# Kernel tuning notes

Measured on AMD Instinct MI355X. Metric: run time of the kernel, lower is better.

## Reference

```python
import jax, jax.numpy as jnp
import numpy as np

B, T_NEW, D_MODEL, H, DH = 8, 512, 1024, 16, 64
CACHED = 2048
T_TOTAL = CACHED + T_NEW  # static padded total length (last batch item is full)


def setup_inputs() -> dict:
    key = jax.random.key(0)
    ks = jax.random.split(key, 16)
    x_new = jax.random.normal(ks[0], (B, T_NEW, D_MODEL), jnp.float32)
    past_lengths = jax.random.randint(ks[1], (B,), CACHED // 2, CACHED)
    past_lengths = past_lengths.at[-1].set(CACHED).astype(jnp.int32)
    new_counts = jax.random.randint(ks[2], (B,), 1, T_NEW)
    new_counts = new_counts.at[-1].set(T_NEW).astype(jnp.int32)
    # prefix (left-aligned) valid mask for new tokens, matching how the torch
    # module compacts k_new[b, :, :count] into the cache
    valid_new_mask = jnp.arange(T_NEW)[None, :] < new_counts[:, None]
    total_lengths = past_lengths + new_counts
    key_padding_mask = jnp.arange(T_TOTAL)[None, :] < total_lengths[:, None]
    inv_freq = 1.0 / (10000.0 ** (jnp.arange(0, DH, 2, dtype=jnp.float32) / DH))
    pm = (jnp.arange(CACHED)[None, :] < past_lengths[:, None])[:, None, :, None]
    past_k = jax.random.normal(ks[3], (B, H, CACHED, DH), jnp.float32) * pm
    past_v = jax.random.normal(ks[4], (B, H, CACHED, DH), jnp.float32) * pm
    s = 0.02
    Wq = jax.random.normal(ks[5], (D_MODEL, D_MODEL), jnp.float32) * s
    Wk = jax.random.normal(ks[6], (D_MODEL, D_MODEL), jnp.float32) * s
    Wv = jax.random.normal(ks[7], (D_MODEL, D_MODEL), jnp.float32) * s
    Wo = jax.random.normal(ks[8], (D_MODEL, D_MODEL), jnp.float32) * s
    bq = jnp.zeros((D_MODEL,), jnp.float32)
    bk = jnp.zeros((D_MODEL,), jnp.float32)
    bv = jnp.zeros((D_MODEL,), jnp.float32)
    bo = jnp.zeros((D_MODEL,), jnp.float32)
    return {
        'x_new': x_new, 'inv_freq': inv_freq, 'past_k': past_k, 'past_v': past_v,
        'Wq': Wq, 'bq': bq, 'Wk': Wk, 'bk': bk, 'Wv': Wv, 'bv': bv, 'Wo': Wo, 'bo': bo,
        'key_padding_mask': key_padding_mask, 'past_lengths': past_lengths,
        'valid_new_mask': valid_new_mask,
    }


def _rotate_half(x):
    h = x.shape[-1] // 2
    return jnp.concatenate([-x[..., h:], x[..., :h]], axis=-1)


def reference(x_new, inv_freq, past_k, past_v, Wq, bq, Wk, bk, Wv, bv, Wo, bo,
              key_padding_mask, past_lengths, valid_new_mask):
    Bb, Tn, _ = x_new.shape
    # projections -> [B, H, T_new, DH]
    q = (x_new @ Wq.T + bq).reshape(Bb, Tn, H, DH).transpose(0, 2, 1, 3)
    k_new = (x_new @ Wk.T + bk).reshape(Bb, Tn, H, DH).transpose(0, 2, 1, 3)
    v_new = (x_new @ Wv.T + bv).reshape(Bb, Tn, H, DH).transpose(0, 2, 1, 3)
    # RoPE at absolute positions past_len + step (invalid -> 0)
    steps = jnp.arange(Tn)
    positions = jnp.where(valid_new_mask, past_lengths[:, None] + steps[None, :], 0)
    freqs = positions[..., None].astype(jnp.float32) * inv_freq  # [B, T, DH/2]
    emb = jnp.concatenate([freqs, freqs], axis=-1)
    cos = jnp.cos(emb)[:, None].astype(q.dtype)  # [B, 1, T, DH]
    sin = jnp.sin(emb)[:, None].astype(q.dtype)
    q = q * cos + _rotate_half(q) * sin
    k_new = k_new * cos + _rotate_half(k_new) * sin
    vm = valid_new_mask[:, None, :, None].astype(q.dtype)
    q = q * vm
    k_new = k_new * vm
    v_new = v_new * vm
    # zero cached entries past each item's cached length (matches padded cache)
    pm = (jnp.arange(CACHED)[None, :] < past_lengths[:, None])[:, None, :, None]
    past_k = past_k * pm.astype(past_k.dtype)
    past_v = past_v * pm.astype(past_v.dtype)
    # ragged append: scatter new tokens at [past_len, past_len+count); invalid
    # tokens dumped into an extra slot T_TOTAL that is sliced off
    pos_idx = jnp.where(valid_new_mask, past_lengths[:, None] + steps[None, :], T_TOTAL)
    pad = lambda p: jnp.pad(p, ((0, 0), (0, 0), (0, T_TOTAL + 1 - CACHED), (0, 0)))
    scat = jax.vmap(lambda base, new, idx: base.at[:, idx, :].add(new))
    k_total = scat(pad(past_k), k_new, pos_idx)[:, :, :T_TOTAL]
    v_total = scat(pad(past_v), v_new, pos_idx)[:, :, :T_TOTAL]
    # padded SDPA with key-padding mask
    scores = jnp.einsum('bhqd,bhkd->bhqk', q, k_total) / jnp.sqrt(jnp.asarray(DH, q.dtype))
    scores = jnp.where(key_padding_mask[:, None, None, :], scores, jnp.finfo(scores.dtype).min)
    attn = jax.nn.softmax(scores, axis=-1)
    ctx = jnp.einsum('bhqk,bhkd->bhqd', attn, v_total)
    ctx = ctx.transpose(0, 2, 1, 3).reshape(Bb, Tn, D_MODEL)
    out = (ctx @ Wo.T + bo) * valid_new_mask[..., None].astype(ctx.dtype)
    total_lengths = past_lengths + valid_new_mask.sum(axis=1).astype(past_lengths.dtype)
    return out, k_total, v_total, total_lengths
```

## Files before the change

### kernel.cpp

```cpp
#include <hip/hip_runtime.h>
#include <math.h>

#define B_ 8
#define TN 512
#define DM 1024
#define H_ 16
#define DH 64
#define CACHED_ 2048
#define TT 2560

#define QSC 0.18033688011112042f

typedef __attribute__((ext_vector_type(8))) short bf16x8;
typedef __attribute__((ext_vector_type(4))) float f32x4;

union U16x8 { uint4 u; unsigned short s[8]; };
union U16x4 { uint2 u; unsigned short s[4]; };
union F4 { float4 v; float f[4]; };

__device__ __forceinline__ unsigned short f2b(float x) {
    unsigned u = __float_as_uint(x);
    unsigned r = (u + 0x7FFFu + ((u >> 16) & 1u)) >> 16;
    return (unsigned short)r;
}
__device__ __forceinline__ float b2f(unsigned short v) {
    return __uint_as_float((unsigned)v << 16);
}

__device__ __forceinline__ unsigned cvt_pk_bf16(float lo, float hi) {
    unsigned r;
    asm("v_cvt_pk_bf16_f32 %0, %1, %2" : "=v"(r) : "v"(lo), "v"(hi));
    return r;
}

__device__ __forceinline__ void gload16(const void* g, void* l) {
    __builtin_amdgcn_global_load_lds(
        (const __attribute__((address_space(1))) void*)g,
        (__attribute__((address_space(3))) void*)l, 16, 0, 0);
}

__global__ void cvt_all(const float* __restrict__ x,
                        const float* __restrict__ Wq,
                        const float* __restrict__ Wk,
                        const float* __restrict__ Wv,
                        const float* __restrict__ Wo,
                        unsigned short* __restrict__ Xbf,
                        unsigned short* __restrict__ Wqkvb,
                        unsigned short* __restrict__ Wob,
                        const unsigned char* __restrict__ vnm,
                        const unsigned char* __restrict__ kpm,
                        const int* __restrict__ past_len,
                        int* __restrict__ counts,
                        float* __restrict__ total_out) {
    if (blockIdx.x >= 4096) {
        int b = blockIdx.x - 4096;
        __shared__ int red[256];
        int esz = (kpm[1] | kpm[2] | kpm[3]) ? 1 : 4;
        int s = 0;
        for (int t = threadIdx.x; t < TN; t += 256)
            s += (vnm[(size_t)(b * TN + t) * esz] != 0) ? 1 : 0;
        red[threadIdx.x] = s;
        __syncthreads();
        for (int off = 128; off > 0; off >>= 1) {
            if (threadIdx.x < off) red[threadIdx.x] += red[threadIdx.x + off];
            __syncthreads();
        }
        if (threadIdx.x == 0) {
            counts[b] = red[0];
            total_out[b] = (float)(past_len[b] + red[0]);
        }
        return;
    }
    int i8 = (blockIdx.x * 256 + threadIdx.x) << 3;
    const float* src;
    unsigned short* dst;
    int off;
    if (i8 < (1 << 22)) {
        src = x; off = i8; dst = Xbf + i8;
    } else if (i8 < (1 << 22) + (3 << 20)) {
        int j = i8 - (1 << 22);
        int w = j >> 20;
        src = w == 0 ? Wq : (w == 1 ? Wk : Wv);
        off = j & 0xFFFFF;
        dst = Wqkvb + j;
    } else {
        int j = i8 - ((1 << 22) + (3 << 20));
        src = Wo; off = j; dst = Wob + j;
    }
    float4 a = *(const float4*)(src + off);
    float4 b = *(const float4*)(src + off + 4);
    U16x8 o;
    o.s[0] = f2b(a.x); o.s[1] = f2b(a.y); o.s[2] = f2b(a.z); o.s[3] = f2b(a.w);
    o.s[4] = f2b(b.x); o.s[5] = f2b(b.y); o.s[6] = f2b(b.z); o.s[7] = f2b(b.w);
    *(uint4*)dst = o.u;
}

__device__ __forceinline__ void gemm_core(
    const unsigned short* __restrict__ A, const unsigned short* __restrict__ Bw,
    int K, int m0, int n0, short* As2, short* Bs2, f32x4 acc[4][4]) {
    const int tid = threadIdx.x;
    const int wave = tid >> 6, lane = tid & 63;
    const int wm = wave >> 1, wn = wave & 1;
    const int l15 = lane & 15, lq = lane >> 4;

    const int srow = wave * 16 + (lane >> 2);
    const int sc = (lane & 3) << 3;
    const unsigned short* Ag0 = A + (size_t)(m0 + srow) * K + sc;
    const unsigned short* Ag1 = A + (size_t)(m0 + 64 + srow) * K + sc;
    const unsigned short* Bg0 = Bw + (size_t)(n0 + srow) * K + sc;
    const unsigned short* Bg1 = Bw + (size_t)(n0 + 64 + srow) * K + sc;
    const int d0 = wave * 512;
    const int d1 = 2048 + wave * 512;

    gload16(Ag0, As2 + d0);
    gload16(Ag1, As2 + d1);
    gload16(Bg0, Bs2 + d0);
    gload16(Bg1, Bs2 + d1);

    int cur = 0;
    for (int k0 = 0; k0 < K; k0 += 32) {
        asm volatile("s_waitcnt vmcnt(0)" ::: "memory");
        __builtin_amdgcn_s_barrier();

        int kn = (k0 + 32 < K) ? k0 + 32 : k0;
        short* An = As2 + ((cur ^ 1) << 12);
        short* Bn = Bs2 + ((cur ^ 1) << 12);
        gload16(Ag0 + kn, An + d0);
        gload16(Ag1 + kn, An + d1);
        gload16(Bg0 + kn, Bn + d0);
        gload16(Bg1 + kn, Bn + d1);

        const short* Ac = As2 + (cur << 12);
        const short* Bc = Bs2 + (cur << 12);
        bf16x8 af[4], bf[4];
#pragma unroll
        for (int mi = 0; mi < 4; ++mi)
            af[mi] = *(const bf16x8*)&Ac[(wm * 64 + mi * 16 + l15) * 32 + lq * 8];
#pragma unroll
        for (int ni = 0; ni < 4; ++ni)
            bf[ni] = *(const bf16x8*)&Bc[(wn * 64 + ni * 16 + l15) * 32 + lq * 8];
#pragma unroll
        for (int mi = 0; mi < 4; ++mi)
#pragma unroll
            for (int ni = 0; ni < 4; ++ni)
                acc[mi][ni] = __builtin_amdgcn_mfma_f32_16x16x32_bf16(
                    af[mi], bf[ni], acc[mi][ni], 0, 0, 0);
        cur ^= 1;
    }
}

__global__ __launch_bounds__(256) void gemm_qkv_mfma(
    const unsigned short* __restrict__ Xbf,
    const unsigned short* __restrict__ Wqkv,
    const float* __restrict__ bq, const float* __restrict__ bk,
    const float* __restrict__ bv, const float* __restrict__ inv_freq,
    const int* __restrict__ past_len,
    unsigned short* __restrict__ Qraw, unsigned short* __restrict__ Kraw,
    unsigned short* __restrict__ Vraw) {
    __shared__ __align__(16) short As[2 * 128 * 32];
    __shared__ __align__(16) short Bs[2 * 128 * 32];
    f32x4 acc[4][4] = {};
    const int m0 = blockIdx.y << 7, n0 = blockIdx.x << 7;
    gemm_core(Xbf, Wqkv, DM, m0, n0, As, Bs, acc);

    const int which = n0 >> 10;
    const int tid = threadIdx.x, wave = tid >> 6, lane = tid & 63;
    const int wm = wave >> 1, wn = wave & 1, l15 = lane & 15, lq = lane >> 4;

    if (which == 0) {
        const int bb = m0 >> 9;
        const int pl = past_len[bb];
        const int hh = (n0 + wn * 64) >> 6;
#pragma unroll
        for (int ni = 0; ni < 2; ++ni) {
            int i = ni * 16 + l15;
            int n1 = n0 + wn * 64 + ni * 16 + l15;
            float fi = inv_freq[i];
            float blo = bq[n1], bhi = bq[n1 + 32];
#pragma unroll
            for (int mi = 0; mi < 4; ++mi) {
#pragma unroll
                for (int r = 0; r < 4; ++r) {
                    int m = m0 + wm * 64 + mi * 16 + lq * 4 + r;
                    int t = m & 511;
                    float ang = (float)(pl + t) * fi;
                    float s, c;
                    __sincosf(ang, &s, &c);
                    float x1 = acc[mi][ni][r] + blo;
                    float x2 = acc[mi][ni + 2][r] + bhi;
                    size_t base = ((size_t)(bb * H_ + hh) * TN + t) * DH;
                    Qraw[base + i]      = f2b((x1 * c - x2 * s) * QSC);
                    Qraw[base + i + 32] = f2b((x2 * c + x1 * s) * QSC);
                }
            }
        }
    } else {
        const float* bias = which == 1 ? bk : bv;
        unsigned short* dst = which == 1 ? Kraw : Vraw;
#pragma unroll
        for (int ni = 0; ni < 4; ++ni) {
            int n1 = (n0 & 1023) + wn * 64 + ni * 16 + l15;
            float bb = bias[n1];
            int h = n1 >> 6, dh = n1 & 63;
#pragma unroll
            for (int mi = 0; mi < 4; ++mi) {
#pragma unroll
                for (int r = 0; r < 4; ++r) {
                    int m = m0 + wm * 64 + mi * 16 + lq * 4 + r;
                    int b = m >> 9, t = m & 511;
                    dst[((size_t)(b * H_ + h) * TN + t) * DH + dh] =
                        f2b(acc[mi][ni][r] + bb);
                }
            }
        }
    }
}

__global__ __launch_bounds__(256) void gemm_out_mfma(
    const unsigned short* __restrict__ Ctxb,
    const unsigned short* __restrict__ Wob,
    const float* __restrict__ bo, const int* __restrict__ counts,
    float* __restrict__ Out) {
    __shared__ __align__(16) short As[2 * 128 * 32];
    __shared__ __align__(16) short Bs[2 * 128 * 32];
    f32x4 acc[4][4] = {};
    const int m0 = blockIdx.y << 7, n0 = blockIdx.x << 7;
    gemm_core(Ctxb, Wob, DM, m0, n0, As, Bs, acc);

    const int tid = threadIdx.x, wave = tid >> 6, lane = tid & 63;
    const int wm = wave >> 1, wn = wave & 1, l15 = lane & 15, lq = lane >> 4;
    const int cnt = counts[m0 >> 9];
#pragma unroll
    for (int mi = 0; mi < 4; ++mi) {
#pragma unroll
        for (int r = 0; r < 4; ++r) {
            int m = m0 + wm * 64 + mi * 16 + lq * 4 + r;
            int t = m & 511;
            bool valid = t < cnt;
#pragma unroll
            for (int ni = 0; ni < 4; ++ni) {
                int n = n0 + wn * 64 + ni * 16 + l15;
                Out[(size_t)m * DM + n] = valid ? acc[mi][ni][r] + bo[n] : 0.f;
            }
        }
    }
}

__global__ void build_kv(const float* __restrict__ past_k,
                         const float* __restrict__ past_v,
                         const unsigned short* __restrict__ Kraw,
                         const unsigned short* __restrict__ Vraw,
                         const float* __restrict__ inv_freq,
                         const int* __restrict__ past_len,
                         const int* __restrict__ counts,
                         float* __restrict__ Ko, float* __restrict__ Vo,
                         unsigned short* __restrict__ Kb16,
                         unsigned short* __restrict__ Vb16) {
    int idx = blockIdx.x * 256 + threadIdx.x;
    int i = idx & 7;
    int p = idx >> 3;
    int h = blockIdx.y, bz = blockIdx.z;
    int pl = past_len[bz], cnt = counts[bz];
    int dh = i << 2;
    size_t obase = ((size_t)(bz * H_ + h) * TT + p) * DH;
    F4 k1, k2, v1, v2;
    if (p < pl) {
        size_t ib = ((size_t)(bz * H_ + h) * CACHED_ + p) * DH;
        k1.v = *(const float4*)(past_k + ib + dh);
        k2.v = *(const float4*)(past_k + ib + dh + 32);
        v1.v = *(const float4*)(past_v + ib + dh);
        v2.v = *(const float4*)(past_v + ib + dh + 32);
    } else if (p < pl + cnt) {
        int t = p - pl;
        size_t ib = ((size_t)(bz * H_ + h) * TN + t) * DH;
        U16x4 ka, kc, va, vc;
        ka.u = *(const uint2*)(Kraw + ib + dh);
        kc.u = *(const uint2*)(Kraw + ib + dh + 32);
        va.u = *(const uint2*)(Vraw + ib + dh);
        vc.u = *(const uint2*)(Vraw + ib + dh + 32);
#pragma unroll
        for (int j = 0; j < 4; ++j) {
            float ang = (float)p * inv_freq[dh + j];
            float s, c;
            __sincosf(ang, &s, &c);
            float x1 = b2f(ka.s[j]), x2 = b2f(kc.s[j]);
            k1.f[j] = x1 * c - x2 * s;
            k2.f[j] = x2 * c + x1 * s;
            v1.f[j] = b2f(va.s[j]);
            v2.f[j] = b2f(vc.s[j]);
        }
    } else {
        k1.v = k2.v = v1.v = v2.v = make_float4(0.f, 0.f, 0.f, 0.f);
    }
    *(float4*)(Ko + obase + dh) = k1.v;
    *(float4*)(Ko + obase + dh + 32) = k2.v;
    *(float4*)(Vo + obase + dh) = v1.v;
    *(float4*)(Vo + obase + dh + 32) = v2.v;
    U16x4 o;
#pragma unroll
    for (int j = 0; j < 4; ++j) o.s[j] = f2b(k1.f[j]);
    *(uint2*)(Kb16 + obase + dh) = o.u;
#pragma unroll
    for (int j = 0; j < 4; ++j) o.s[j] = f2b(k2.f[j]);
    *(uint2*)(Kb16 + obase + dh + 32) = o.u;
#pragma unroll
    for (int j = 0; j < 4; ++j) o.s[j] = f2b(v1.f[j]);
    *(uint2*)(Vb16 + obase + dh) = o.u;
#pragma unroll
    for (int j = 0; j < 4; ++j) o.s[j] = f2b(v2.f[j]);
    *(uint2*)(Vb16 + obase + dh + 32) = o.u;
}

__global__ __launch_bounds__(512) void attn_mfma(
    const unsigned short* __restrict__ Qbf,
    const unsigned short* __restrict__ Kb,
    const unsigned short* __restrict__ Vb,
    const int* __restrict__ past_len, const int* __restrict__ counts,
    unsigned short* __restrict__ Ctxb) {
    const int j = blockIdx.x;
    const int xcd = j & 7;
    const int tloc = j >> 3;
    const int qt = tloc & 3;
    const int p = ((tloc >> 2) << 3) | xcd;
    const int b = p >> 4, h = p & 15;

    const int tid = threadIdx.x;
    const int wave = tid >> 6, lane = tid & 63;
    const int l15 = lane & 15, lq = lane >> 4;

    __shared__ __align__(16) short Qs[8192];
    __shared__ __align__(16) short Ks[2][4096];
    __shared__ __align__(16) short Vt[4096];
    __shared__ __align__(16) short Pb[8192];

    const size_t qbase = ((size_t)(b * H_ + h) * TN + qt * 128) * DH;
    const size_t kbase = (size_t)(b * H_ + h) * TT * DH;

    const int total = past_len[b] + counts[b];
    const int ntiles = (total + 63) >> 6;

    const int dA = tid;
    const int krA = (dA >> 7) * 16 + ((dA & 15) ^ ((dA >> 4) & 7));
    const int kcA = ((dA >> 4) & 7) << 3;
    const unsigned short* KgA = Kb + kbase + (size_t)krA * DH + kcA;
    const int kdoffA = wave * 512;

    gload16(KgA, &Ks[0][kdoffA]);

    const int kp = tid & 31;
    const int dh4 = (tid >> 5) << 2;
    const int kc = kp >> 2, ko2 = (kp & 3) << 1;
    const unsigned short* Vg = Vb + kbase + (size_t)(2 * kp) * DH + dh4;
    uint2 vr0 = *(const uint2*)Vg;
    uint2 vr1 = *(const uint2*)(Vg + DH);

#pragma unroll
    for (int jj = 0; jj < 2; ++jj) {
        int e = tid + (jj << 9);
        int row = e >> 3, c = e & 7;
        *(uint4*)&Qs[(((row >> 4) * 8 + c) * 16 + ((row & 15) ^ c)) * 8] =
            *(const uint4*)(Qbf + qbase + row * 64 + c * 8);
    }
    __syncthreads();
    const int c0 = lq, c1 = 4 + lq;
    bf16x8 qa0 = *(const bf16x8*)&Qs[((wave * 8 + c0) * 16 + (l15 ^ c0)) * 8];
    bf16x8 qa1 = *(const bf16x8*)&Qs[((wave * 8 + c1) * 16 + (l15 ^ c1)) * 8];

    float rsum[4] = {0.f, 0.f, 0.f, 0.f};
    f32x4 O[4] = {};
    unsigned short* Pw = (unsigned short*)(Pb + wave * 1024);
    const int pc0 = l15 >> 3, pwo = l15 & 7;

    int cur = 0;
    for (int kt = 0; kt < ntiles; ++kt) {
        asm volatile("s_waitcnt vmcnt(0)" ::: "memory");
        __builtin_amdgcn_s_barrier();

        {
            U16x4 a, cc;
            a.u = vr0;
            cc.u = vr1;
#pragma unroll
            for (int jj = 0; jj < 4; ++jj) {
                int dh = dh4 + jj;
                unsigned pk = (unsigned)a.s[jj] | ((unsigned)cc.s[jj] << 16);
                *(unsigned*)&Vt[((((dh >> 4) * 8 + kc) * 16) + ((dh & 15) ^ kc)) * 8 + ko2] = pk;
            }
        }
        {
            int ktn = (kt + 1 < ntiles) ? kt + 1 : kt;
            gload16(KgA + (size_t)ktn * 64 * DH, &Ks[cur ^ 1][kdoffA]);
            vr0 = *(const uint2*)(Vg + (size_t)ktn * 64 * DH);
            vr1 = *(const uint2*)(Vg + (size_t)ktn * 64 * DH + DH);
        }

        asm volatile("s_waitcnt lgkmcnt(0)" ::: "memory");
        __builtin_amdgcn_s_barrier();
        __builtin_amdgcn_sched_barrier(0);

        const short* Kcur = Ks[cur];
        f32x4 S[4];
        __builtin_amdgcn_s_setprio(1);
#pragma unroll
        for (int nt = 0; nt < 4; ++nt) {
            f32x4 acc = {};
            bf16x8 kb0 = *(const bf16x8*)&Kcur[((nt * 8 + c0) * 16 + (l15 ^ c0)) * 8];
            acc = __builtin_amdgcn_mfma_f32_16x16x32_bf16(qa0, kb0, acc, 0, 0, 0);
            bf16x8 kb1 = *(const bf16x8*)&Kcur[((nt * 8 + c1) * 16 + (l15 ^ c1)) * 8];
            acc = __builtin_amdgcn_mfma_f32_16x16x32_bf16(qa1, kb1, acc, 0, 0, 0);
            S[nt] = acc;
        }
        __builtin_amdgcn_s_setprio(0);

        int limit = total - (kt << 6);
        if (limit < 64) {
#pragma unroll
            for (int nt = 0; nt < 4; ++nt) {
                bool ok = nt * 16 + l15 < limit;
#pragma unroll
                for (int r = 0; r < 4; ++r) S[nt][r] = ok ? S[nt][r] : -1e30f;
            }
        }

#pragma unroll
        for (int nt = 0; nt < 4; ++nt) {
            const int pc = nt * 2 + pc0;
#pragma unroll
            for (int rr = 0; rr < 2; ++rr) {
                float p0 = __builtin_amdgcn_exp2f(S[nt][2 * rr]);
                float p1 = __builtin_amdgcn_exp2f(S[nt][2 * rr + 1]);
                rsum[2 * rr] += p0;
                rsum[2 * rr + 1] += p1;
                unsigned pk = cvt_pk_bf16(p0, p1);
                int row0 = lq * 4 + 2 * rr;
                int row1 = row0 + 1;
                Pw[(pc * 16 + (row0 ^ pc)) * 8 + pwo] = (unsigned short)pk;
                Pw[(pc * 16 + (row1 ^ pc)) * 8 + pwo] = (unsigned short)(pk >> 16);
            }
        }
        asm volatile("s_waitcnt lgkmcnt(0)" ::: "memory");

        bf16x8 pa0 = *(const bf16x8*)&Pw[(c0 * 16 + (l15 ^ c0)) * 8];
        bf16x8 pa1 = *(const bf16x8*)&Pw[(c1 * 16 + (l15 ^ c1)) * 8];
        __builtin_amdgcn_s_setprio(1);
#pragma unroll
        for (int nt = 0; nt < 4; ++nt) {
            bf16x8 vb0 = *(const bf16x8*)&Vt[((nt * 8 + c0) * 16 + (l15 ^ c0)) * 8];
            O[nt] = __builtin_amdgcn_mfma_f32_16x16x32_bf16(pa0, vb0, O[nt], 0, 0, 0);
            bf16x8 vb1 = *(const bf16x8*)&Vt[((nt * 8 + c1) * 16 + (l15 ^ c1)) * 8];
            O[nt] = __builtin_amdgcn_mfma_f32_16x16x32_bf16(pa1, vb1, O[nt], 0, 0, 0);
        }
        __builtin_amdgcn_s_setprio(0);
        cur ^= 1;
    }

#pragma unroll
    for (int off = 1; off < 16; off <<= 1)
#pragma unroll
        for (int r = 0; r < 4; ++r) rsum[r] += __shfl_xor(rsum[r], off);

#pragma unroll
    for (int r = 0; r < 4; ++r) {
        float inv = 1.f / rsum[r];
        int t = qt * 128 + wave * 16 + lq * 4 + r;
        size_t mbase = ((size_t)(b * TN + t)) * DM + h * DH;
#pragma unroll
        for (int nt = 0; nt < 4; ++nt)
            Ctxb[mbase + nt * 16 + l15] = f2b(O[nt][r] * inv);
    }
}

extern "C" void kernel_launch(void* const* d_in, const int* in_sizes, int n_in,
                              void* d_out, int out_size, void* d_ws, size_t ws_size,
                              hipStream_t stream) {
    const float* x_new    = (const float*)d_in[0];
    const float* inv_freq = (const float*)d_in[1];
    const float* past_k   = (const float*)d_in[2];
    const float* past_v   = (const float*)d_in[3];
    const float* Wq = (const float*)d_in[4];
    const float* bq = (const float*)d_in[5];
    const float* Wk = (const float*)d_in[6];
    const float* bk = (const float*)d_in[7];
    const float* Wv = (const float*)d_in[8];
    const float* bv = (const float*)d_in[9];
    const float* Wo = (const float*)d_in[10];
    const float* bo = (const float*)d_in[11];
    const unsigned char* kpm = (const unsigned char*)d_in[12];
    const int* past_len      = (const int*)d_in[13];
    const unsigned char* vnm = (const unsigned char*)d_in[14];

    float* out      = (float*)d_out;
    float* k_total  = out + (size_t)B_ * TN * DM;
    float* v_total  = k_total + (size_t)B_ * H_ * TT * DH;
    float* total_out = v_total + (size_t)B_ * H_ * TT * DH;

    const size_t NQ = (size_t)B_ * TN * DM;
    const size_t NKV = (size_t)B_ * H_ * TT * DH;

    int* counts = (int*)d_ws;
    unsigned short* Xbf   = (unsigned short*)((char*)d_ws + 256);
    unsigned short* Wqkvb = Xbf + NQ;
    unsigned short* Wob   = Wqkvb + (size_t)3 * DM * DM;
    unsigned short* Qraw  = Wob + (size_t)DM * DM;
    unsigned short* Kraw  = Qraw + NQ;
    unsigned short* Vraw  = Kraw + NQ;
    unsigned short* Ctxb  = Vraw + NQ;
    unsigned short* Kb16  = Ctxb + NQ;
    unsigned short* Vb16  = Kb16 + NKV;

    cvt_all<<<4104, 256, 0, stream>>>(x_new, Wq, Wk, Wv, Wo, Xbf, Wqkvb, Wob,
                                      vnm, kpm, past_len, counts, total_out);

    gemm_qkv_mfma<<<dim3(24, 32), 256, 0, stream>>>(
        Xbf, Wqkvb, bq, bk, bv, inv_freq, past_len, Qraw, Kraw, Vraw);
    build_kv<<<dim3((TT * 8) / 256, H_, B_), 256, 0, stream>>>(
        past_k, past_v, Kraw, Vraw, inv_freq, past_len, counts,
        k_total, v_total, Kb16, Vb16);
    attn_mfma<<<512, 512, 0, stream>>>(Qraw, Kb16, Vb16,
                                       past_len, counts, Ctxb);
    gemm_out_mfma<<<dim3(8, 32), 256, 0, stream>>>(Ctxb, Wob, bo, counts, out);
}
```

Baseline: 496.9 us.

## Split attention over KV halves and merge partial results in a separate kernel

Attention now splits each (batch, head, q-tile) across two blocks, each handling half of the KV tiles, and writes unnormalized fp32 partial outputs and row sums to workspace. A new merge kernel sums the two partials, normalizes, and writes the bf16 context. The aim is to double the block count and balance ragged sequence lengths across CUs. The Q and P shared buffers are merged to cut LDS use, launch bounds now request higher occupancy, and the setprio hints are dropped. The cost is extra fp32 global traffic and one more kernel launch. Merging without a running max is valid only because scores are not max-subtracted, the same as in the code before.

```diff
diff --git a/kernel.cpp b/kernel.cpp
--- a/kernel.cpp
+++ b/kernel.cpp
@@ -10,6 +10,8 @@
 #define TT 2560
 
 #define QSC 0.18033688011112042f
+#define OHALF 4194304
+#define RHALF 65536
 
 typedef __attribute__((ext_vector_type(8))) short bf16x8;
 typedef __attribute__((ext_vector_type(4))) float f32x4;
@@ -311,33 +313,38 @@
     *(uint2*)(Vb16 + obase + dh + 32) = o.u;
 }
 
-__global__ __launch_bounds__(512) void attn_mfma(
+__global__ __launch_bounds__(512, 8) void attn_split(
     const unsigned short* __restrict__ Qbf,
     const unsigned short* __restrict__ Kb,
     const unsigned short* __restrict__ Vb,
     const int* __restrict__ past_len, const int* __restrict__ counts,
-    unsigned short* __restrict__ Ctxb) {
+    float* __restrict__ Opart,
+    float* __restrict__ Rpart) {
     const int j = blockIdx.x;
     const int xcd = j & 7;
-    const int tloc = j >> 3;
-    const int qt = tloc & 3;
-    const int p = ((tloc >> 2) << 3) | xcd;
+    const int sub = (j >> 3) & 7;
+    const int qt = sub & 3;
+    const int half = sub >> 2;
+    const int pg = j >> 6;
+    const int p = pg * 8 + xcd;
     const int b = p >> 4, h = p & 15;
 
     const int tid = threadIdx.x;
     const int wave = tid >> 6, lane = tid & 63;
     const int l15 = lane & 15, lq = lane >> 4;
 
-    __shared__ __align__(16) short Qs[8192];
     __shared__ __align__(16) short Ks[2][4096];
     __shared__ __align__(16) short Vt[4096];
-    __shared__ __align__(16) short Pb[8192];
+    __shared__ __align__(16) short PQ[8192];
 
     const size_t qbase = ((size_t)(b * H_ + h) * TN + qt * 128) * DH;
     const size_t kbase = (size_t)(b * H_ + h) * TT * DH;
 
     const int total = past_len[b] + counts[b];
     const int ntiles = (total + 63) >> 6;
+    const int nth = (ntiles + 1) >> 1;
+    const int kt0 = half * nth;
+    const int kt1 = (kt0 + nth < ntiles) ? kt0 + nth : ntiles;
 
     const int dA = tid;
     const int krA = (dA >> 7) * 16 + ((dA & 15) ^ ((dA >> 4) & 7));
@@ -345,34 +352,34 @@
     const unsigned short* KgA = Kb + kbase + (size_t)krA * DH + kcA;
     const int kdoffA = wave * 512;
 
-    gload16(KgA, &Ks[0][kdoffA]);
+    gload16(KgA + (size_t)kt0 * 64 * DH, &Ks[0][kdoffA]);
 
     const int kp = tid & 31;
     const int dh4 = (tid >> 5) << 2;
     const int kc = kp >> 2, ko2 = (kp & 3) << 1;
     const unsigned short* Vg = Vb + kbase + (size_t)(2 * kp) * DH + dh4;
-    uint2 vr0 = *(const uint2*)Vg;
-    uint2 vr1 = *(const uint2*)(Vg + DH);
+    uint2 vr0 = *(const uint2*)(Vg + (size_t)kt0 * 64 * DH);
+    uint2 vr1 = *(const uint2*)(Vg + (size_t)kt0 * 64 * DH + DH);
 
 #pragma unroll
     for (int jj = 0; jj < 2; ++jj) {
         int e = tid + (jj << 9);
         int row = e >> 3, c = e & 7;
-        *(uint4*)&Qs[(((row >> 4) * 8 + c) * 16 + ((row & 15) ^ c)) * 8] =
+        *(uint4*)&PQ[(((row >> 4) * 8 + c) * 16 + ((row & 15) ^ c)) * 8] =
             *(const uint4*)(Qbf + qbase + row * 64 + c * 8);
     }
     __syncthreads();
     const int c0 = lq, c1 = 4 + lq;
-    bf16x8 qa0 = *(const bf16x8*)&Qs[((wave * 8 + c0) * 16 + (l15 ^ c0)) * 8];
-    bf16x8 qa1 = *(const bf16x8*)&Qs[((wave * 8 + c1) * 16 + (l15 ^ c1)) * 8];
+    bf16x8 qa0 = *(const bf16x8*)&PQ[((wave * 8 + c0) * 16 + (l15 ^ c0)) * 8];
+    bf16x8 qa1 = *(const bf16x8*)&PQ[((wave * 8 + c1) * 16 + (l15 ^ c1)) * 8];
 
     float rsum[4] = {0.f, 0.f, 0.f, 0.f};
     f32x4 O[4] = {};
-    unsigned short* Pw = (unsigned short*)(Pb + wave * 1024);
+    unsigned short* Pw = (unsigned short*)(PQ + wave * 1024);
     const int pc0 = l15 >> 3, pwo = l15 & 7;
 
     int cur = 0;
-    for (int kt = 0; kt < ntiles; ++kt) {
+    for (int kt = kt0; kt < kt1; ++kt) {
         asm volatile("s_waitcnt vmcnt(0)" ::: "memory");
         __builtin_amdgcn_s_barrier();
 
@@ -388,7 +395,7 @@
             }
         }
         {
-            int ktn = (kt + 1 < ntiles) ? kt + 1 : kt;
+            int ktn = (kt + 1 < kt1) ? kt + 1 : kt;
             gload16(KgA + (size_t)ktn * 64 * DH, &Ks[cur ^ 1][kdoffA]);
             vr0 = *(const uint2*)(Vg + (size_t)ktn * 64 * DH);
             vr1 = *(const uint2*)(Vg + (size_t)ktn * 64 * DH + DH);
@@ -400,7 +407,6 @@
 
         const short* Kcur = Ks[cur];
         f32x4 S[4];
-        __builtin_amdgcn_s_setprio(1);
 #pragma unroll
         for (int nt = 0; nt < 4; ++nt) {
             f32x4 acc = {};
@@ -410,7 +416,6 @@
             acc = __builtin_amdgcn_mfma_f32_16x16x32_bf16(qa1, kb1, acc, 0, 0, 0);
             S[nt] = acc;
         }
-        __builtin_amdgcn_s_setprio(0);
 
         int limit = total - (kt << 6);
         if (limit < 64) {
@@ -442,7 +447,6 @@
 
         bf16x8 pa0 = *(const bf16x8*)&Pw[(c0 * 16 + (l15 ^ c0)) * 8];
         bf16x8 pa1 = *(const bf16x8*)&Pw[(c1 * 16 + (l15 ^ c1)) * 8];
-        __builtin_amdgcn_s_setprio(1);
 #pragma unroll
         for (int nt = 0; nt < 4; ++nt) {
             bf16x8 vb0 = *(const bf16x8*)&Vt[((nt * 8 + c0) * 16 + (l15 ^ c0)) * 8];
@@ -450,7 +454,6 @@
             bf16x8 vb1 = *(const bf16x8*)&Vt[((nt * 8 + c1) * 16 + (l15 ^ c1)) * 8];
             O[nt] = __builtin_amdgcn_mfma_f32_16x16x32_bf16(pa1, vb1, O[nt], 0, 0, 0);
         }
-        __builtin_amdgcn_s_setprio(0);
         cur ^= 1;
     }
 
@@ -459,15 +462,42 @@
 #pragma unroll
         for (int r = 0; r < 4; ++r) rsum[r] += __shfl_xor(rsum[r], off);
 
+    float* Od = Opart + (size_t)half * OHALF;
+    float* Rd = Rpart + (size_t)half * RHALF;
 #pragma unroll
     for (int r = 0; r < 4; ++r) {
-        float inv = 1.f / rsum[r];
         int t = qt * 128 + wave * 16 + lq * 4 + r;
-        size_t mbase = ((size_t)(b * TN + t)) * DM + h * DH;
+        size_t obase = ((size_t)(b * H_ + h) * TN + t) * DH;
 #pragma unroll
         for (int nt = 0; nt < 4; ++nt)
-            Ctxb[mbase + nt * 16 + l15] = f2b(O[nt][r] * inv);
-    }
+            Od[obase + nt * 16 + l15] = O[nt][r];
+        if (l15 == 0) Rd[(size_t)(b * H_ + h) * TN + t] = rsum[r];
+    }
+}
+
+__global__ __launch_bounds__(256) void attn_merge(
+    const float* __restrict__ Opart, const float* __restrict__ Rpart,
+    unsigned short* __restrict__ Ctxb) {
+    int idx = blockIdx.x * 256 + threadIdx.x;
+    int i8 = idx & 7;
+    int row = idx >> 3;
+    int dh8 = i8 << 3;
+    const float* O0 = Opart + (size_t)row * DH + dh8;
+    const float* O1 = O0 + OHALF;
+    float inv = 1.f / (Rpart[row] + Rpart[RHALF + row]);
+    int t = row & 511, bh = row >> 9;
+    int h = bh & 15, b = bh >> 4;
+    F4 a0, a1, c0, c1;
+    a0.v = *(const float4*)O0;
+    a1.v = *(const float4*)(O0 + 4);
+    c0.v = *(const float4*)O1;
+    c1.v = *(const float4*)(O1 + 4);
+    U16x8 o;
+#pragma unroll
+    for (int jj = 0; jj < 4; ++jj) o.s[jj] = f2b((a0.f[jj] + c0.f[jj]) * inv);
+#pragma unroll
+    for (int jj = 0; jj < 4; ++jj) o.s[4 + jj] = f2b((a1.f[jj] + c1.f[jj]) * inv);
+    *(uint4*)(Ctxb + ((size_t)(b * TN + t)) * DM + h * 64 + dh8) = o.u;
 }
 
 extern "C" void kernel_launch(void* const* d_in, const int* in_sizes, int n_in,
@@ -507,6 +537,8 @@
     unsigned short* Ctxb  = Vraw + NQ;
     unsigned short* Kb16  = Ctxb + NQ;
     unsigned short* Vb16  = Kb16 + NKV;
+    float* Opart = (float*)(Vb16 + NKV);
+    float* Rpart = Opart + 2 * (size_t)OHALF;
 
     cvt_all<<<4104, 256, 0, stream>>>(x_new, Wq, Wk, Wv, Wo, Xbf, Wqkvb, Wob,
                                       vnm, kpm, past_len, counts, total_out);
@@ -516,7 +548,8 @@
     build_kv<<<dim3((TT * 8) / 256, H_, B_), 256, 0, stream>>>(
         past_k, past_v, Kraw, Vraw, inv_freq, past_len, counts,
         k_total, v_total, Kb16, Vb16);
-    attn_mfma<<<512, 512, 0, stream>>>(Qraw, Kb16, Vb16,
-                                       past_len, counts, Ctxb);
+    attn_split<<<1024, 512, 0, stream>>>(Qraw, Kb16, Vb16,
+                                         past_len, counts, Opart, Rpart);
+    attn_merge<<<(B_ * H_ * TN * 8) / 256, 256, 0, stream>>>(Opart, Rpart, Ctxb);
     gemm_out_mfma<<<dim3(8, 32), 256, 0, stream>>>(Ctxb, Wob, bo, counts, out);
 }
```

Result: slower. 653.3 us (+31.5%).
